# Performance work log

Hardware: AMD Instinct MI355X
Metric: run time of the kernel (lower is better)

Reference implementation:

```python
import jax, jax.numpy as jnp
import numpy as np

B, H, W, DIM = 2, 64, 64, 128
NH = 4
HD = DIM // NH
KS = 7
DIL = 2
SCALE = HD ** -0.5


def _natten_idx(L, k, dil):
    """Per-position neighborhood start + rpb start (NATTEN semantics), as gather index tables."""
    ns = k // 2
    starts = np.empty(L, np.int32)
    pbs = np.empty(L, np.int32)
    for i in range(L):
        if dil <= 1:
            s = max(i - ns, 0) + (i + ns >= L) * (L - i - ns - 1)
            p = ns + (i < ns) * (ns - i) + (i + ns >= L) * (L - i - 1 - ns)
        else:
            if i - ns * dil < 0:
                s = i % dil
                p = k - 1 - (i // dil)
            elif i + ns * dil >= L:
                imodd = i % dil
                a = (L // dil) * dil
                b = L - a
                if imodd < b:
                    s = L - b + imodd - 2 * ns * dil
                else:
                    s = a + imodd - k * dil
                p = (L - i - 1) // dil
            else:
                s = i - ns * dil
                p = ns
        starts[i] = s
        pbs[i] = p
    key_idx = starts[:, None] + dil * np.arange(k, dtype=np.int32)  # [L, k] key positions
    pb_idx = pbs[:, None] + np.arange(k, dtype=np.int32)            # [L, k] rpb positions
    return key_idx, pb_idx


def setup_inputs() -> dict:
    key = jax.random.key(0)
    ks = jax.random.split(key, 12)
    shp = (B, H, W, DIM)
    q = jax.random.normal(ks[0], shp, jnp.float32)
    k = jax.random.normal(ks[1], shp, jnp.float32)
    v = jax.random.normal(ks[2], shp, jnp.float32)
    def lin(kk):
        return jax.random.normal(kk, (DIM, DIM), jnp.float32) * (DIM ** -0.5)
    Wq, Wk, Wv, Wo = lin(ks[3]), lin(ks[4]), lin(ks[5]), lin(ks[6])
    bq = jnp.zeros((DIM,), jnp.float32)
    bk = jnp.zeros((DIM,), jnp.float32)
    bv = jnp.zeros((DIM,), jnp.float32)
    bo = jnp.zeros((DIM,), jnp.float32)
    rpb = jax.random.normal(ks[7], (NH, 2 * KS - 1, 2 * KS - 1), jnp.float32) * 0.02
    return {"q": q, "k": k, "v": v, "Wq": Wq, "bq": bq, "Wk": Wk, "bk": bk,
            "Wv": Wv, "bv": bv, "rpb": rpb, "Wo": Wo, "bo": bo}


def _forward(q, k, v, Wq, bq, Wk, bk, Wv, bv, rpb, Wo, bo):
    Bc, Hc, Wc, C = q.shape
    ii, pi = _natten_idx(Hc, KS, DIL)   # [H, K]
    jj, pj = _natten_idx(Wc, KS, DIL)   # [W, K]

    def heads(x, Wm, bm):
        # [B,H,W,C] -> [B,NH,H,W,HD]
        return (x @ Wm + bm).reshape(Bc, Hc, Wc, NH, HD).transpose(0, 3, 1, 2, 4)

    qh = heads(q, Wq, bq) * SCALE
    kh = heads(k, Wk, bk)
    vh = heads(v, Wv, bv)

    # Gather KxK dilated neighborhoods: [B,NH,H,K,W,K,HD]
    knbr = kh[:, :, ii][:, :, :, :, jj]
    vnbr = vh[:, :, ii][:, :, :, :, jj]

    # attention logits per pixel over its KxK neighborhood: [B,NH,H,W,K,K]
    attn = jnp.einsum('bnhwd,bnhkwld->bnhwkl', qh, knbr)
    # relative position bias lookup: [NH,H,K,W,K] -> [NH,H,W,K,K]
    bias = rpb[:, pi][:, :, :, pj].transpose(0, 1, 3, 2, 4)
    attn = attn + bias[None]

    attn = jax.nn.softmax(attn.reshape(Bc, NH, Hc, Wc, KS * KS), axis=-1)
    attn = attn.reshape(Bc, NH, Hc, Wc, KS, KS)

    out = jnp.einsum('bnhwkl,bnhkwld->bnhwd', attn, vnbr)
    out = out.transpose(0, 2, 3, 1, 4).reshape(Bc, Hc, Wc, C)
    return out @ Wo + bo


def reference(q, k, v, Wq, bq, Wk, bk, Wv, bv, rpb, Wo, bo):
    return _forward(q, k, v, Wq, bq, Wk, bk, Wv, bv, rpb, Wo, bo)
```

## Files before the change

### kernel.cpp

```cpp
#include <hip/hip_runtime.h>
#include <hip/hip_bf16.h>
#include <math.h>

#define BB 2
#define HH 64
#define WW 64
#define DIMC 128
#define NH 4
#define HD 32
#define KS 7
#define DIL 2
#define NPIX (BB * HH * WW)
#define SCALE 0.17677669529663687f

typedef short bf16x8 __attribute__((ext_vector_type(8)));
typedef float f32x4  __attribute__((ext_vector_type(4)));

__device__ __forceinline__ short bf16r(float f) {
    union { float f; unsigned u; } x; x.f = f;
    unsigned r = x.u + 0x7FFF + ((x.u >> 16) & 1);
    return (short)(r >> 16);
}
__device__ __forceinline__ float uasf(unsigned u) {
    union { unsigned u; float f; } x; x.u = u; return x.f;
}

__global__ __launch_bounds__(256) void prep_w(
    const float* __restrict__ Wq, const float* __restrict__ Wk,
    const float* __restrict__ Wv, const float* __restrict__ Wo,
    short* __restrict__ Wt)
{
    const int z  = blockIdx.x >> 2;
    const int ks = blockIdx.x & 3;
    const float* W = (z == 0) ? Wq : (z == 1) ? Wk : (z == 2) ? Wv : Wo;

    __shared__ short T[32][136];
    const int t = threadIdx.x;
    const float4* Wg = (const float4*)(W + ks * 32 * 128);

    float4 xv[4];
#pragma unroll
    for (int u = 0; u < 4; ++u) xv[u] = Wg[u * 256 + t];
#pragma unroll
    for (int u = 0; u < 4; ++u) {
        const int e = u * 256 + t;
        const int r = e >> 5;
        const int c = (e & 31) * 4;
        short4 s4;
        s4.x = bf16r(xv[u].x); s4.y = bf16r(xv[u].y);
        s4.z = bf16r(xv[u].z); s4.w = bf16r(xv[u].w);
        *(short4*)&T[r][c] = s4;
    }
    __syncthreads();

    const int c = t >> 1;
    const int h = (t & 1) * 16;
    bf16x8 lo, hi;
#pragma unroll
    for (int i = 0; i < 8; ++i) { lo[i] = T[h + i][c]; hi[i] = T[h + 8 + i][c]; }
    short* outp = Wt + z * 16384 + c * 128 + ks * 32 + h;
    *(bf16x8*)(outp)     = lo;
    *(bf16x8*)(outp + 8) = hi;
}

__global__ __launch_bounds__(256) void qkv_mfma(
    const float* __restrict__ q, const float* __restrict__ k,
    const float* __restrict__ v, const short* __restrict__ Wt,
    const float* __restrict__ bq, const float* __restrict__ bk,
    const float* __restrict__ bv,
    float* __restrict__ qh, short* __restrict__ khb, short* __restrict__ vhb)
{
    const int z = blockIdx.y;
    const float* X    = (z == 0) ? q  : (z == 1) ? k  : v;
    const float* bias = (z == 0) ? bq : (z == 1) ? bk : bv;
    const short* Wz   = Wt + z * 16384;

    const int t    = threadIdx.x;
    const int wv   = t >> 6;
    const int lane = t & 63;
    const int lr   = lane & 15;
    const int lg   = lane >> 4;
    const int row0 = blockIdx.x * 32 + (wv & 1) * 16;
    const int col0 = (wv >> 1) * 64;

    bf16x8 bfr[16];
#pragma unroll
    for (int nt = 0; nt < 4; ++nt) {
        const short* wrow = Wz + (col0 + nt * 16 + lr) * 128 + lg * 8;
#pragma unroll
        for (int kk = 0; kk < 4; ++kk)
            bfr[nt * 4 + kk] = *(const bf16x8*)(wrow + kk * 32);
    }

    const float* xrow = X + (size_t)(row0 + lr) * 128 + lg * 8;
    bf16x8 a[4];
#pragma unroll
    for (int kk = 0; kk < 4; ++kk) {
        const float4 x0 = *(const float4*)(xrow + kk * 32);
        const float4 x1 = *(const float4*)(xrow + kk * 32 + 4);
        bf16x8 av;
        av[0] = bf16r(x0.x); av[1] = bf16r(x0.y);
        av[2] = bf16r(x0.z); av[3] = bf16r(x0.w);
        av[4] = bf16r(x1.x); av[5] = bf16r(x1.y);
        av[6] = bf16r(x1.z); av[7] = bf16r(x1.w);
        a[kk] = av;
    }

#pragma unroll
    for (int nt = 0; nt < 4; ++nt) {
        const int col = col0 + nt * 16 + lr;
        f32x4 acc = {0.f, 0.f, 0.f, 0.f};
#pragma unroll
        for (int kk = 0; kk < 4; ++kk)
            acc = __builtin_amdgcn_mfma_f32_16x16x32_bf16(a[kk], bfr[nt * 4 + kk], acc, 0, 0, 0);
        const float bc = bias[col];
        if (z == 0) {
#pragma unroll
            for (int jj = 0; jj < 4; ++jj)
                qh[(size_t)(row0 + lg * 4 + jj) * 128 + col] = (acc[jj] + bc) * SCALE;
        } else {
            short* Yb = (z == 1) ? khb : vhb;
#pragma unroll
            for (int jj = 0; jj < 4; ++jj)
                Yb[(size_t)(row0 + lg * 4 + jj) * 128 + col] = bf16r(acc[jj] + bc);
        }
    }
}

__device__ __forceinline__ void natten_idx(int i, int& s, int& p)
{
    if (i < 6) {
        s = i & 1;
        p = 6 - (i >> 1);
    } else if (i >= 58) {
        s = 50 + (i & 1);
        p = (63 - i) >> 1;
    } else {
        s = i - 6;
        p = 3;
    }
}

__global__ __launch_bounds__(256) void natten_out(
    const float* __restrict__ qh, const short* __restrict__ khb,
    const short* __restrict__ vhb, const float* __restrict__ rpb,
    const short* __restrict__ Wt, const float* __restrict__ bo,
    float* __restrict__ out)
{
    __shared__ short attS[16][136];

    const int blk  = blockIdx.x;
    const int work = (blk & 7) * 64 + (blk >> 3);
    const int t    = threadIdx.x;

    {
        const int lane4 = t & 3;
        const int n  = (t >> 2) & 3;
        const int p  = t >> 4;
        const int g  = work * 16 + p;
        const int j  = g & 63;
        const int i  = (g >> 6) & 63;
        const int b  = g >> 12;

        int si, pi0, sj, pj0;
        natten_idx(i, si, pi0);
        natten_idx(j, sj, pj0);

        const int coff = n * 32 + lane4 * 8;
        const size_t pixb = (size_t)(b * 4096 + i * 64 + j);
        const float4 q0 = *(const float4*)(qh + pixb * 128 + coff);
        const float4 q1 = *(const float4*)(qh + pixb * 128 + coff + 4);

        const float* rp = rpb + n * 169;

        float m = -1e30f, l = 0.0f;
        float o[8] = {0.f, 0.f, 0.f, 0.f, 0.f, 0.f, 0.f, 0.f};

#pragma unroll
        for (int ki = 0; ki < 7; ++ki) {
            const int iy = si + 2 * ki;
            const size_t rowbase = ((size_t)(b * 4096 + iy * 64)) * 128 + coff;
            const float* rrow = rp + (pi0 + ki) * 13 + pj0;

            float d[7];
#pragma unroll
            for (int kj = 0; kj < 7; ++kj) {
                const int ix = sj + 2 * kj;
                const uint4 kv = *(const uint4*)(khb + rowbase + (size_t)ix * 128);
                float dd =      q0.x * uasf(kv.x << 16);
                dd = fmaf(q0.y, uasf(kv.x & 0xFFFF0000u), dd);
                dd = fmaf(q0.z, uasf(kv.y << 16), dd);
                dd = fmaf(q0.w, uasf(kv.y & 0xFFFF0000u), dd);
                dd = fmaf(q1.x, uasf(kv.z << 16), dd);
                dd = fmaf(q1.y, uasf(kv.z & 0xFFFF0000u), dd);
                dd = fmaf(q1.z, uasf(kv.w << 16), dd);
                dd = fmaf(q1.w, uasf(kv.w & 0xFFFF0000u), dd);
                d[kj] = dd;
            }
#pragma unroll
            for (int kj = 0; kj < 7; ++kj) d[kj] += __shfl_xor(d[kj], 1);
#pragma unroll
            for (int kj = 0; kj < 7; ++kj) d[kj] += __shfl_xor(d[kj], 2);
#pragma unroll
            for (int kj = 0; kj < 7; ++kj) d[kj] += rrow[kj];

            const float g01 = fmaxf(d[0], d[1]);
            const float g23 = fmaxf(d[2], d[3]);
            const float g45 = fmaxf(d[4], d[5]);
            const float gm  = fmaxf(fmaxf(g01, g23), fmaxf(g45, d[6]));
            const float mn  = fmaxf(m, gm);
            const float corr = __expf(m - mn);
            m = mn;
            l *= corr;
#pragma unroll
            for (int e = 0; e < 8; ++e) o[e] *= corr;

#pragma unroll
            for (int kj = 0; kj < 7; ++kj) {
                const float pe = __expf(d[kj] - m);
                d[kj] = pe;
                l += pe;
            }

#pragma unroll
            for (int kj = 0; kj < 7; ++kj) {
                const int ix = sj + 2 * kj;
                const uint4 vv = *(const uint4*)(vhb + rowbase + (size_t)ix * 128);
                const float pe = d[kj];
                o[0] = fmaf(pe, uasf(vv.x << 16),          o[0]);
                o[1] = fmaf(pe, uasf(vv.x & 0xFFFF0000u),  o[1]);
                o[2] = fmaf(pe, uasf(vv.y << 16),          o[2]);
                o[3] = fmaf(pe, uasf(vv.y & 0xFFFF0000u),  o[3]);
                o[4] = fmaf(pe, uasf(vv.z << 16),          o[4]);
                o[5] = fmaf(pe, uasf(vv.z & 0xFFFF0000u),  o[5]);
                o[6] = fmaf(pe, uasf(vv.w << 16),          o[6]);
                o[7] = fmaf(pe, uasf(vv.w & 0xFFFF0000u),  o[7]);
            }
        }

        const float inv = 1.0f / l;
        bf16x8 ow;
#pragma unroll
        for (int e = 0; e < 8; ++e) ow[e] = bf16r(o[e] * inv);
        *(bf16x8*)&attS[p][coff] = ow;
    }

    __syncthreads();

    {
        const int wv   = t >> 6;
        const int lane = t & 63;
        const int lr   = lane & 15;
        const int lg   = lane >> 4;
        const int col0 = wv * 32;
        const short* Wz = Wt + 3 * 16384;

        bf16x8 bfr[8];
#pragma unroll
        for (int nt = 0; nt < 2; ++nt) {
            const short* wrow = Wz + (col0 + nt * 16 + lr) * 128 + lg * 8;
#pragma unroll
            for (int kk = 0; kk < 4; ++kk)
                bfr[nt * 4 + kk] = *(const bf16x8*)(wrow + kk * 32);
        }
        bf16x8 a[4];
#pragma unroll
        for (int kk = 0; kk < 4; ++kk)
            a[kk] = *(const bf16x8*)&attS[lr][kk * 32 + lg * 8];

#pragma unroll
        for (int nt = 0; nt < 2; ++nt) {
            const int col = col0 + nt * 16 + lr;
            f32x4 acc = {0.f, 0.f, 0.f, 0.f};
#pragma unroll
            for (int kk = 0; kk < 4; ++kk)
                acc = __builtin_amdgcn_mfma_f32_16x16x32_bf16(a[kk], bfr[nt * 4 + kk], acc, 0, 0, 0);
            const float bc = bo[col];
#pragma unroll
            for (int jj = 0; jj < 4; ++jj)
                out[(size_t)(work * 16 + lg * 4 + jj) * 128 + col] = acc[jj] + bc;
        }
    }
}

extern "C" void kernel_launch(void* const* d_in, const int* in_sizes, int n_in,
                              void* d_out, int out_size, void* d_ws, size_t ws_size,
                              hipStream_t stream)
{
    const float* q   = (const float*)d_in[0];
    const float* k   = (const float*)d_in[1];
    const float* v   = (const float*)d_in[2];
    const float* Wq  = (const float*)d_in[3];
    const float* bq  = (const float*)d_in[4];
    const float* Wk  = (const float*)d_in[5];
    const float* bk  = (const float*)d_in[6];
    const float* Wv  = (const float*)d_in[7];
    const float* bv  = (const float*)d_in[8];
    const float* rpb = (const float*)d_in[9];
    const float* Wo  = (const float*)d_in[10];
    const float* bo  = (const float*)d_in[11];

    float* ws   = (float*)d_ws;
    float* qh   = ws;
    short* khb  = (short*)(ws + (size_t)NPIX * 128);
    short* vhb  = khb + (size_t)NPIX * 128;
    short* Wt   = vhb + (size_t)NPIX * 128;
    float* out  = (float*)d_out;

    hipLaunchKernelGGL(prep_w, dim3(16), dim3(256), 0, stream, Wq, Wk, Wv, Wo, Wt);

    hipLaunchKernelGGL(qkv_mfma, dim3(256, 3), dim3(256), 0, stream,
                       q, k, v, Wt, bq, bk, bv, qh, khb, vhb);

    hipLaunchKernelGGL(natten_out, dim3(512), dim3(256), 0, stream,
                       qh, khb, vhb, rpb, Wt, bo, out);
}
```

Baseline: 35.20 us.

## Split neighborhood rows across two thread halves and merge softmax partials

Doubles the natten_out block to 512 threads, so each pixel/head's 7 neighborhood rows are split between two thread groups (4 rows each, with the eighth row masked). Their online-softmax states are merged through lane shuffles. The output projection is re-tiled so each of the 8 waves computes 16 columns. This shortens the serial dependency chain per thread and raises parallelism. The cost is one wasted masked row of K/V loads and extra shuffle/merge work.

```diff
diff --git a/kernel.cpp b/kernel.cpp
--- a/kernel.cpp
+++ b/kernel.cpp
@@ -141,7 +141,7 @@
     }
 }
 
-__global__ __launch_bounds__(256) void natten_out(
+__global__ __launch_bounds__(512, 4) void natten_out(
     const float* __restrict__ qh, const short* __restrict__ khb,
     const short* __restrict__ vhb, const float* __restrict__ rpb,
     const short* __restrict__ Wt, const float* __restrict__ bo,
@@ -155,12 +155,13 @@
 
     {
         const int lane4 = t & 3;
-        const int n  = (t >> 2) & 3;
-        const int p  = t >> 4;
-        const int g  = work * 16 + p;
-        const int j  = g & 63;
-        const int i  = (g >> 6) & 63;
-        const int b  = g >> 12;
+        const int n   = (t >> 2) & 3;
+        const int kih = (t >> 4) & 1;
+        const int p   = t >> 5;
+        const int g   = work * 16 + p;
+        const int j   = g & 63;
+        const int i   = (g >> 6) & 63;
+        const int b   = g >> 12;
 
         int si, pi0, sj, pj0;
         natten_idx(i, si, pi0);
@@ -177,10 +178,13 @@
         float o[8] = {0.f, 0.f, 0.f, 0.f, 0.f, 0.f, 0.f, 0.f};
 
 #pragma unroll
-        for (int ki = 0; ki < 7; ++ki) {
-            const int iy = si + 2 * ki;
+        for (int r = 0; r < 4; ++r) {
+            const int ki  = kih * 4 + r;
+            const int kic = (ki > 6) ? 6 : ki;
+            const bool masked = (ki == 7);
+            const int iy = si + 2 * kic;
             const size_t rowbase = ((size_t)(b * 4096 + iy * 64)) * 128 + coff;
-            const float* rrow = rp + (pi0 + ki) * 13 + pj0;
+            const float* rrow = rp + (pi0 + kic) * 13 + pj0;
 
             float d[7];
 #pragma unroll
@@ -202,7 +206,8 @@
 #pragma unroll
             for (int kj = 0; kj < 7; ++kj) d[kj] += __shfl_xor(d[kj], 2);
 #pragma unroll
-            for (int kj = 0; kj < 7; ++kj) d[kj] += rrow[kj];
+            for (int kj = 0; kj < 7; ++kj)
+                d[kj] = masked ? -1e30f : (d[kj] + rrow[kj]);
 
             const float g01 = fmaxf(d[0], d[1]);
             const float g23 = fmaxf(d[2], d[3]);
@@ -238,11 +243,25 @@
             }
         }
 
-        const float inv = 1.0f / l;
-        bf16x8 ow;
-#pragma unroll
-        for (int e = 0; e < 8; ++e) ow[e] = bf16r(o[e] * inv);
-        *(bf16x8*)&attS[p][coff] = ow;
+        const float mo  = __shfl_xor(m, 16);
+        const float lo_ = __shfl_xor(l, 16);
+        const float mm  = fmaxf(m, mo);
+        const float f   = __expf(m - mm);
+        const float fo  = __expf(mo - mm);
+        float lm = l * f + lo_ * fo;
+#pragma unroll
+        for (int e = 0; e < 8; ++e) {
+            const float oo = __shfl_xor(o[e], 16);
+            o[e] = o[e] * f + oo * fo;
+        }
+
+        const float inv = 1.0f / lm;
+        if (kih == 0) {
+            bf16x8 ow;
+#pragma unroll
+            for (int e = 0; e < 8; ++e) ow[e] = bf16r(o[e] * inv);
+            *(bf16x8*)&attS[p][coff] = ow;
+        }
     }
 
     __syncthreads();
@@ -252,34 +271,30 @@
         const int lane = t & 63;
         const int lr   = lane & 15;
         const int lg   = lane >> 4;
-        const int col0 = wv * 32;
+        const int col0 = wv * 16;
         const short* Wz = Wt + 3 * 16384;
 
-        bf16x8 bfr[8];
-#pragma unroll
-        for (int nt = 0; nt < 2; ++nt) {
-            const short* wrow = Wz + (col0 + nt * 16 + lr) * 128 + lg * 8;
-#pragma unroll
-            for (int kk = 0; kk < 4; ++kk)
-                bfr[nt * 4 + kk] = *(const bf16x8*)(wrow + kk * 32);
-        }
+        bf16x8 bfr[4];
+        const short* wrow = Wz + (col0 + lr) * 128 + lg * 8;
+#pragma unroll
+        for (int kk = 0; kk < 4; ++kk)
+            bfr[kk] = *(const bf16x8*)(wrow + kk * 32);
+
         bf16x8 a[4];
 #pragma unroll
         for (int kk = 0; kk < 4; ++kk)
             a[kk] = *(const bf16x8*)&attS[lr][kk * 32 + lg * 8];
 
-#pragma unroll
-        for (int nt = 0; nt < 2; ++nt) {
-            const int col = col0 + nt * 16 + lr;
-            f32x4 acc = {0.f, 0.f, 0.f, 0.f};
-#pragma unroll
-            for (int kk = 0; kk < 4; ++kk)
-                acc = __builtin_amdgcn_mfma_f32_16x16x32_bf16(a[kk], bfr[nt * 4 + kk], acc, 0, 0, 0);
-            const float bc = bo[col];
-#pragma unroll
-            for (int jj = 0; jj < 4; ++jj)
-                out[(size_t)(work * 16 + lg * 4 + jj) * 128 + col] = acc[jj] + bc;
-        }
+        f32x4 acc = {0.f, 0.f, 0.f, 0.f};
+#pragma unroll
+        for (int kk = 0; kk < 4; ++kk)
+            acc = __builtin_amdgcn_mfma_f32_16x16x32_bf16(a[kk], bfr[kk], acc, 0, 0, 0);
+
+        const int col = col0 + lr;
+        const float bc = bo[col];
+#pragma unroll
+        for (int jj = 0; jj < 4; ++jj)
+            out[(size_t)(work * 16 + lg * 4 + jj) * 128 + col] = acc[jj] + bc;
     }
 }
 
@@ -312,6 +327,6 @@
     hipLaunchKernelGGL(qkv_mfma, dim3(256, 3), dim3(256), 0, stream,
                        q, k, v, Wt, bq, bk, bv, qh, khb, vhb);
 
-    hipLaunchKernelGGL(natten_out, dim3(512), dim3(256), 0, stream,
+    hipLaunchKernelGGL(natten_out, dim3(512), dim3(512), 0, stream,
                        qh, khb, vhb, rpb, Wt, bo, out);
 }
```

Result: slower. 70.71 us (+100.9%).

## Stage shared K neighborhood tile in LDS for each block's 16-pixel row strip

Applied to the files above, without the earlier changes.

Each block now handles 16 consecutive pixels in one image row and cooperatively loads the union of their K neighborhoods (7 rows by 28 columns by 128 channels, bf16) into shared memory before the attention loop. Per-thread K reads then come from LDS instead of repeated global or L2 loads, since neighboring pixels share most of their keys. V still streams from global memory. The change costs about 53 KB of LDS per block, which limits occupancy, and adds a prologue load plus an extra barrier before the shared buffer is reused for the output tile.

```diff
diff --git a/kernel.cpp b/kernel.cpp
--- a/kernel.cpp
+++ b/kernel.cpp
@@ -147,31 +147,60 @@
     const short* __restrict__ Wt, const float* __restrict__ bo,
     float* __restrict__ out)
 {
-    __shared__ short attS[16][136];
+    __shared__ short smem[7 * 28 * 136];
+    short (*kls)[28][136] = (short (*)[28][136])smem;
+    short (*attS)[136]    = (short (*)[136])smem;
 
     const int blk  = blockIdx.x;
     const int work = (blk & 7) * 64 + (blk >> 3);
     const int t    = threadIdx.x;
 
+    const int j0 = (work & 3) * 16;
+    const int i_ = (work >> 2) & 63;
+    const int b_ = work >> 8;
+
+    int si_, pi_, sj0, pj_;
+    natten_idx(i_, si_, pi_);
+    natten_idx(j0, sj0, pj_);
+    const int colbase = sj0;
+
+    {
+        const size_t bbase = (size_t)(b_ * 4096) * 128;
+#pragma unroll
+        for (int u = t; u < 3136; u += 256) {
+            const int row  = u >> 4;
+            const int ch16 = (u & 15) * 8;
+            const int ki   = row / 28;
+            const int c    = row - ki * 28;
+            int col = colbase + c;
+            col = (col > 63) ? 63 : col;
+            const int iy = si_ + 2 * ki;
+            const uint4 kv = *(const uint4*)(khb + bbase + (size_t)(iy * 64 + col) * 128 + ch16);
+            *(uint4*)&kls[ki][c][ch16] = kv;
+        }
+    }
+    __syncthreads();
+
+    float o0, o1, o2, o3, o4, o5, o6, o7, invl;
+    int p_, coff_;
+
     {
         const int lane4 = t & 3;
-        const int n  = (t >> 2) & 3;
-        const int p  = t >> 4;
-        const int g  = work * 16 + p;
-        const int j  = g & 63;
-        const int i  = (g >> 6) & 63;
-        const int b  = g >> 12;
+        const int n   = (t >> 2) & 3;
+        const int p   = t >> 4;
+        const int j   = j0 + p;
 
         int si, pi0, sj, pj0;
-        natten_idx(i, si, pi0);
+        natten_idx(i_, si, pi0);
         natten_idx(j, sj, pj0);
 
         const int coff = n * 32 + lane4 * 8;
-        const size_t pixb = (size_t)(b * 4096 + i * 64 + j);
+        const size_t pixb = (size_t)(b_ * 4096 + i_ * 64 + j);
         const float4 q0 = *(const float4*)(qh + pixb * 128 + coff);
         const float4 q1 = *(const float4*)(qh + pixb * 128 + coff + 4);
 
         const float* rp = rpb + n * 169;
+        const int cj0 = sj - colbase;
 
         float m = -1e30f, l = 0.0f;
         float o[8] = {0.f, 0.f, 0.f, 0.f, 0.f, 0.f, 0.f, 0.f};
@@ -179,14 +208,13 @@
 #pragma unroll
         for (int ki = 0; ki < 7; ++ki) {
             const int iy = si + 2 * ki;
-            const size_t rowbase = ((size_t)(b * 4096 + iy * 64)) * 128 + coff;
+            const size_t rowbase = ((size_t)(b_ * 4096 + iy * 64)) * 128 + coff;
             const float* rrow = rp + (pi0 + ki) * 13 + pj0;
 
             float d[7];
 #pragma unroll
             for (int kj = 0; kj < 7; ++kj) {
-                const int ix = sj + 2 * kj;
-                const uint4 kv = *(const uint4*)(khb + rowbase + (size_t)ix * 128);
+                const uint4 kv = *(const uint4*)&kls[ki][cj0 + 2 * kj][coff];
                 float dd =      q0.x * uasf(kv.x << 16);
                 dd = fmaf(q0.y, uasf(kv.x & 0xFFFF0000u), dd);
                 dd = fmaf(q0.z, uasf(kv.y << 16), dd);
@@ -238,11 +266,21 @@
             }
         }
 
-        const float inv = 1.0f / l;
+        invl = 1.0f / l;
+        o0 = o[0]; o1 = o[1]; o2 = o[2]; o3 = o[3];
+        o4 = o[4]; o5 = o[5]; o6 = o[6]; o7 = o[7];
+        p_ = p; coff_ = coff;
+    }
+
+    __syncthreads();
+
+    {
         bf16x8 ow;
-#pragma unroll
-        for (int e = 0; e < 8; ++e) ow[e] = bf16r(o[e] * inv);
-        *(bf16x8*)&attS[p][coff] = ow;
+        ow[0] = bf16r(o0 * invl); ow[1] = bf16r(o1 * invl);
+        ow[2] = bf16r(o2 * invl); ow[3] = bf16r(o3 * invl);
+        ow[4] = bf16r(o4 * invl); ow[5] = bf16r(o5 * invl);
+        ow[6] = bf16r(o6 * invl); ow[7] = bf16r(o7 * invl);
+        *(bf16x8*)&attS[p_][coff_] = ow;
     }
 
     __syncthreads();
```

Result: slower. 38.61 us (+9.7%).

## Fuse weight transpose/bf16 conversion into consumer kernels via shared-memory staging

Applied to the files above, without the earlier changes.

Removes the separate prep_w launch. Each qkv and output block now loads its fp32 weight matrix, converts it to bf16, transposes it into LDS and reads MFMA B-fragments from there. This drops one kernel launch and its dependency. In exchange, every block redundantly reads the 64KB weight, does scalar strided LDS writes that may bank-conflict, and uses about 35KB more LDS per block, which may reduce occupancy.

```diff
diff --git a/kernel.cpp b/kernel.cpp
--- a/kernel.cpp
+++ b/kernel.cpp
@@ -25,72 +25,47 @@
     union { unsigned u; float f; } x; x.u = u; return x.f;
 }
 
-__global__ __launch_bounds__(256) void prep_w(
-    const float* __restrict__ Wq, const float* __restrict__ Wk,
-    const float* __restrict__ Wv, const float* __restrict__ Wo,
-    short* __restrict__ Wt)
-{
-    const int z  = blockIdx.x >> 2;
-    const int ks = blockIdx.x & 3;
-    const float* W = (z == 0) ? Wq : (z == 1) ? Wk : (z == 2) ? Wv : Wo;
-
-    __shared__ short T[32][136];
-    const int t = threadIdx.x;
-    const float4* Wg = (const float4*)(W + ks * 32 * 128);
-
-    float4 xv[4];
-#pragma unroll
-    for (int u = 0; u < 4; ++u) xv[u] = Wg[u * 256 + t];
-#pragma unroll
-    for (int u = 0; u < 4; ++u) {
-        const int e = u * 256 + t;
-        const int r = e >> 5;
-        const int c = (e & 31) * 4;
-        short4 s4;
-        s4.x = bf16r(xv[u].x); s4.y = bf16r(xv[u].y);
-        s4.z = bf16r(xv[u].z); s4.w = bf16r(xv[u].w);
-        *(short4*)&T[r][c] = s4;
-    }
-    __syncthreads();
-
-    const int c = t >> 1;
-    const int h = (t & 1) * 16;
-    bf16x8 lo, hi;
-#pragma unroll
-    for (int i = 0; i < 8; ++i) { lo[i] = T[h + i][c]; hi[i] = T[h + 8 + i][c]; }
-    short* outp = Wt + z * 16384 + c * 128 + ks * 32 + h;
-    *(bf16x8*)(outp)     = lo;
-    *(bf16x8*)(outp + 8) = hi;
+__device__ __forceinline__ void stage_wT(const float* __restrict__ W,
+                                         short* __restrict__ Wls, int t)
+{
+#pragma unroll
+    for (int e = 0; e < 16; ++e) {
+        const int idx4 = e * 256 + t;
+        const float4 w = *(const float4*)(W + idx4 * 4);
+        const int k = idx4 >> 5;
+        const int c = (idx4 & 31) * 4;
+        Wls[(c + 0) * 136 + k] = bf16r(w.x);
+        Wls[(c + 1) * 136 + k] = bf16r(w.y);
+        Wls[(c + 2) * 136 + k] = bf16r(w.z);
+        Wls[(c + 3) * 136 + k] = bf16r(w.w);
+    }
 }
 
 __global__ __launch_bounds__(256) void qkv_mfma(
     const float* __restrict__ q, const float* __restrict__ k,
-    const float* __restrict__ v, const short* __restrict__ Wt,
+    const float* __restrict__ v,
+    const float* __restrict__ Wq, const float* __restrict__ Wk,
+    const float* __restrict__ Wv,
     const float* __restrict__ bq, const float* __restrict__ bk,
     const float* __restrict__ bv,
     float* __restrict__ qh, short* __restrict__ khb, short* __restrict__ vhb)
 {
+    __shared__ short Wls[128 * 136];
+
     const int z = blockIdx.y;
     const float* X    = (z == 0) ? q  : (z == 1) ? k  : v;
+    const float* W    = (z == 0) ? Wq : (z == 1) ? Wk : Wv;
     const float* bias = (z == 0) ? bq : (z == 1) ? bk : bv;
-    const short* Wz   = Wt + z * 16384;
 
     const int t    = threadIdx.x;
+    stage_wT(W, Wls, t);
+
     const int wv   = t >> 6;
     const int lane = t & 63;
     const int lr   = lane & 15;
     const int lg   = lane >> 4;
     const int row0 = blockIdx.x * 32 + (wv & 1) * 16;
     const int col0 = (wv >> 1) * 64;
-
-    bf16x8 bfr[16];
-#pragma unroll
-    for (int nt = 0; nt < 4; ++nt) {
-        const short* wrow = Wz + (col0 + nt * 16 + lr) * 128 + lg * 8;
-#pragma unroll
-        for (int kk = 0; kk < 4; ++kk)
-            bfr[nt * 4 + kk] = *(const bf16x8*)(wrow + kk * 32);
-    }
 
     const float* xrow = X + (size_t)(row0 + lr) * 128 + lg * 8;
     bf16x8 a[4];
@@ -106,6 +81,17 @@
         a[kk] = av;
     }
 
+    __syncthreads();
+
+    bf16x8 bfr[16];
+#pragma unroll
+    for (int nt = 0; nt < 4; ++nt) {
+        const short* wrow = Wls + (col0 + nt * 16 + lr) * 136 + lg * 8;
+#pragma unroll
+        for (int kk = 0; kk < 4; ++kk)
+            bfr[nt * 4 + kk] = *(const bf16x8*)(wrow + kk * 32);
+    }
+
 #pragma unroll
     for (int nt = 0; nt < 4; ++nt) {
         const int col = col0 + nt * 16 + lr;
@@ -144,23 +130,26 @@
 __global__ __launch_bounds__(256) void natten_out(
     const float* __restrict__ qh, const short* __restrict__ khb,
     const short* __restrict__ vhb, const float* __restrict__ rpb,
-    const short* __restrict__ Wt, const float* __restrict__ bo,
+    const float* __restrict__ Wo, const float* __restrict__ bo,
     float* __restrict__ out)
 {
+    __shared__ short WoT[128 * 136];
     __shared__ short attS[16][136];
 
     const int blk  = blockIdx.x;
     const int work = (blk & 7) * 64 + (blk >> 3);
     const int t    = threadIdx.x;
 
+    stage_wT(Wo, WoT, t);
+
     {
         const int lane4 = t & 3;
-        const int n  = (t >> 2) & 3;
-        const int p  = t >> 4;
-        const int g  = work * 16 + p;
-        const int j  = g & 63;
-        const int i  = (g >> 6) & 63;
-        const int b  = g >> 12;
+        const int n   = (t >> 2) & 3;
+        const int p   = t >> 4;
+        const int g   = work * 16 + p;
+        const int j   = g & 63;
+        const int i   = (g >> 6) & 63;
+        const int b   = g >> 12;
 
         int si, pi0, sj, pj0;
         natten_idx(i, si, pi0);
@@ -253,12 +242,11 @@
         const int lr   = lane & 15;
         const int lg   = lane >> 4;
         const int col0 = wv * 32;
-        const short* Wz = Wt + 3 * 16384;
 
         bf16x8 bfr[8];
 #pragma unroll
         for (int nt = 0; nt < 2; ++nt) {
-            const short* wrow = Wz + (col0 + nt * 16 + lr) * 128 + lg * 8;
+            const short* wrow = WoT + (col0 + nt * 16 + lr) * 136 + lg * 8;
 #pragma unroll
             for (int kk = 0; kk < 4; ++kk)
                 bfr[nt * 4 + kk] = *(const bf16x8*)(wrow + kk * 32);
@@ -304,14 +292,11 @@
     float* qh   = ws;
     short* khb  = (short*)(ws + (size_t)NPIX * 128);
     short* vhb  = khb + (size_t)NPIX * 128;
-    short* Wt   = vhb + (size_t)NPIX * 128;
     float* out  = (float*)d_out;
 
-    hipLaunchKernelGGL(prep_w, dim3(16), dim3(256), 0, stream, Wq, Wk, Wv, Wo, Wt);
-
     hipLaunchKernelGGL(qkv_mfma, dim3(256, 3), dim3(256), 0, stream,
-                       q, k, v, Wt, bq, bk, bv, qh, khb, vhb);
+                       q, k, v, Wq, Wk, Wv, bq, bk, bv, qh, khb, vhb);
 
     hipLaunchKernelGGL(natten_out, dim3(512), dim3(256), 0, stream,
-                       qh, khb, vhb, rpb, Wt, bo, out);
-}
+                       qh, khb, vhb, rpb, Wo, bo, out);
+}
```

Result: slower. 39.15 us (+11.2%).
